# Kernel optimization log

Measured on AMD Instinct MI355X. Metric: run time of the kernel, lower is better.

Reference implementation:

```python
import jax, jax.numpy as jnp
import numpy as np
from jax.scipy.special import logsumexp

PAD = 0  # NlpContext().padding_idx


def setup_inputs() -> dict:
    key = jax.random.key(0)
    k1, k2, k3 = jax.random.split(key, 3)
    B, S, L = 4, 1024, 128
    pred = jax.random.normal(k1, (B, S, L), dtype=jnp.float32)
    # labels in [1, L): no token equals PAD -> mask is all-zero, non_pad_length == S
    gt = jax.random.randint(k2, (B, S), 1, L)
    transition = jax.random.normal(k3, (L, L), dtype=jnp.float32)
    return {"pred": pred, "gt": gt, "transition": transition}


def _crf_loss(pred, gt, transition):
    # Faithful translation of LinearCRFLoss.forward (including the alpha
    # broadcasting behaviour of the original torch loop).
    mask = (gt == PAD).astype(pred.dtype)                 # (B,S), all-zero here
    logp = jax.nn.log_softmax(pred, -1) * (1.0 - mask)[:, :, None]  # (B,S,L)
    trans = jax.nn.log_softmax(transition, -1)            # (L,L)

    # posterior_t[b,i,j] = log_softmax_j( logp[b,t,i] + trans[i,j]*(1-mask[b,t]) )
    post = jax.nn.log_softmax(
        logp[:, :, :, None] + trans[None, None] * (1.0 - mask)[:, :, None, None],
        axis=-1,
    )  # (B,S,L,L)

    # t = 1: alpha has shape (B,L,1) in the original -> broadcasts over 'to'
    # axis j; reduce (logsumexp) over the 'from' axis i.
    alpha = logsumexp(post[:, 1] + logp[:, 0, :, None], axis=1)  # (B,L)
    # t >= 2: alpha has shape (B,1,L) in the original -> broadcasts over the
    # 'from' axis i, so it factors out of the logsumexp:
    #   alpha_t[j] = alpha_{t-1}[j] + lse_i post_t[i,j]
    # which telescopes into a single sum over t (identical math, vectorized).
    alpha = alpha + logsumexp(post[:, 2:], axis=2).sum(axis=1)   # (B,L)
    forward_score = logsumexp(alpha, axis=-1)                    # (B,)

    # gold path score (non_pad_length == S since there is no padding)
    emit = jnp.take_along_axis(logp, gt[:, :, None], axis=2)[..., 0].sum(-1)  # (B,)
    tr = trans[gt[:, :-1], gt[:, 1:]].sum(-1)                                  # (B,)
    gold = emit + tr
    return -(gold - forward_score).mean()


def reference(pred, gt, transition):
    return _crf_loss(pred, gt, transition)
```

## Files before the change

kernel.cpp:

```cpp
#include <hip/hip_runtime.h>
#include <hip/hip_bf16.h>
#include <math.h>

#define BB 4
#define SS 1024
#define LL 128


__global__ __launch_bounds__(256) void crf_rows_kernel(
    const float* __restrict__ pred,
    const int* __restrict__ gt,
    const float* __restrict__ transition,
    float* __restrict__ ws_part,
    float* __restrict__ ws_elp,
    float* __restrict__ ws_trans)
{
    const int wave = threadIdx.x >> 6;
    const int lane = threadIdx.x & 63;
    const int row0 = blockIdx.x * 16;

    int gi[4];
    #pragma unroll
    for (int it = 0; it < 4; ++it) gi[it] = gt[row0 + it * 4 + wave];
    float2 v[4];
    #pragma unroll
    for (int it = 0; it < 4; ++it)
        v[it] = ((const float2*)(pred + (size_t)(row0 + it * 4 + wave) * LL))[lane];
    const bool do_trans = (blockIdx.x < LL) && (wave == 0);
    float2 tv;
    if (do_trans) tv = ((const float2*)(transition + blockIdx.x * LL))[lane];

    float local = 0.f;
    #pragma unroll
    for (int it = 0; it < 4; ++it) {
        float m = fmaxf(v[it].x, v[it].y);
        #pragma unroll
        for (int off = 32; off > 0; off >>= 1) m = fmaxf(m, __shfl_xor(m, off));
        float s = __expf(v[it].x - m) + __expf(v[it].y - m);
        #pragma unroll
        for (int off = 32; off > 0; off >>= 1) s += __shfl_xor(s, off);
        const float lse = m + __logf(s);

        const int g = gi[it];
        const float hold = (g & 1) ? v[it].y : v[it].x;
        local += __shfl(hold, g >> 1) - lse;

        if (it == 0 && wave == 0 && (blockIdx.x & 63) == 0) {
            const int b = blockIdx.x >> 6;
            ws_elp[b * LL + 2 * lane]     = __expf(v[0].x - lse);
            ws_elp[b * LL + 2 * lane + 1] = __expf(v[0].y - lse);
        }
    }

    if (do_trans) {
        float m = fmaxf(tv.x, tv.y);
        #pragma unroll
        for (int off = 32; off > 0; off >>= 1) m = fmaxf(m, __shfl_xor(m, off));
        float s = __expf(tv.x - m) + __expf(tv.y - m);
        #pragma unroll
        for (int off = 32; off > 0; off >>= 1) s += __shfl_xor(s, off);
        const float lse = m + __logf(s);
        float2 o; o.x = tv.x - lse; o.y = tv.y - lse;
        ((float2*)(ws_trans + blockIdx.x * LL))[lane] = o;
    }

    __shared__ float red[4];
    if (lane == 0) red[wave] = local;
    __syncthreads();
    if (threadIdx.x == 0)
        ws_part[blockIdx.x] = red[0] + red[1] + red[2] + red[3];
}

#define PADL (LL + 4)
__global__ __launch_bounds__(512) void crf_finish_kernel(
    const int* __restrict__ gt,
    const float* __restrict__ ws_part,
    const float* __restrict__ ws_elp,
    const float* __restrict__ ws_trans,
    float* __restrict__ out)
{
    __shared__ float tr_s[LL][PADL];
    __shared__ float elp_s[BB][LL];
    __shared__ float pc[4][LL];
    __shared__ float pa[4][BB][LL];
    __shared__ float emit_s[BB];
    __shared__ float wred[8];
    __shared__ float fm[8], fs[8];

    const int tid  = threadIdx.x;
    const int lane = tid & 63;
    const int wave = tid >> 6;

    const int gb = tid >> 7;
    const int t0 = tid & (LL - 1);
    int gf[8], gs[8];
    {
        const int* gtb = gt + gb * SS;
        #pragma unroll
        for (int k = 0; k < 8; ++k) {
            const int t = t0 + k * LL;
            const bool val = (t < SS - 1);
            gf[k] = val ? gtb[t]     : 0;
            gs[k] = val ? gtb[t + 1] : 0;
        }
    }

    #pragma unroll
    for (int k = 0; k < 8; ++k) {
        const int e = (tid + k * 512) * 4;
        const int i = e >> 7, j = e & (LL - 1);
        *(float4*)&tr_s[i][j] = ((const float4*)ws_trans)[e >> 2];
    }
    elp_s[tid >> 7][tid & (LL - 1)] = ws_elp[tid];
    if (wave < BB) {
        float p = ws_part[wave * 64 + lane];
        #pragma unroll
        for (int off = 32; off > 0; off >>= 1) p += __shfl_xor(p, off);
        if (lane == 0) emit_s[wave] = p;
    }
    __syncthreads();

    {
        const int sub = tid >> 7;
        const int j   = tid & (LL - 1);
        float sc = 0.f, s0 = 0.f, s1 = 0.f, s2 = 0.f, s3 = 0.f;
        #pragma unroll
        for (int k = 0; k < 32; ++k) {
            const int i = sub * 32 + k;
            const float e = __expf(tr_s[i][j]);
            sc += e;
            s0 += e * elp_s[0][i];
            s1 += e * elp_s[1][i];
            s2 += e * elp_s[2][i];
            s3 += e * elp_s[3][i];
        }
        pc[sub][j] = sc;
        pa[sub][0][j] = s0; pa[sub][1][j] = s1;
        pa[sub][2][j] = s2; pa[sub][3][j] = s3;
    }
    {
        float g = 0.f;
        #pragma unroll
        for (int k = 0; k < 8; ++k) {
            const int t = t0 + k * LL;
            if (t < SS - 1) g += tr_s[gf[k]][gs[k]];
        }
        #pragma unroll
        for (int off = 32; off > 0; off >>= 1) g += __shfl_xor(g, off);
        if (lane == 0) wred[wave] = g;
    }
    __syncthreads();

    {
        const int b = tid >> 7;
        const int j = tid & (LL - 1);
        const float csum = pc[0][j] + pc[1][j] + pc[2][j] + pc[3][j];
        const float asum = pa[0][b][j] + pa[1][b][j] + pa[2][b][j] + pa[3][b][j];
        const float alpha = __logf(asum) + (float)(SS - 2) * __logf(csum);

        float wm = alpha;
        #pragma unroll
        for (int off = 32; off > 0; off >>= 1) wm = fmaxf(wm, __shfl_xor(wm, off));
        float wsum = __expf(alpha - wm);
        #pragma unroll
        for (int off = 32; off > 0; off >>= 1) wsum += __shfl_xor(wsum, off);
        if (lane == 0) { fm[wave] = wm; fs[wave] = wsum; }
    }
    __syncthreads();

    if (tid < BB) {
        const float m0 = fm[2 * tid], m1 = fm[2 * tid + 1];
        const float mm = fmaxf(m0, m1);
        const float fwd = mm + __logf(fs[2 * tid] * __expf(m0 - mm)
                                    + fs[2 * tid + 1] * __expf(m1 - mm));
        const float gold = wred[2 * tid] + wred[2 * tid + 1];
        fm[tid] = emit_s[tid] + gold - fwd;
    }
    __syncthreads();
    if (tid == 0)
        out[0] = -(fm[0] + fm[1] + fm[2] + fm[3]) * (1.0f / BB);
}

extern "C" void kernel_launch(void* const* d_in, const int* in_sizes, int n_in,
                              void* d_out, int out_size, void* d_ws, size_t ws_size,
                              hipStream_t stream) {
    const float* pred       = (const float*)d_in[0];
    const int*   gt         = (const int*)d_in[1];
    const float* transition = (const float*)d_in[2];
    float* out = (float*)d_out;

    float* ws_part  = (float*)d_ws;
    float* ws_elp   = ws_part + 256;
    float* ws_trans = ws_part + 768;

    crf_rows_kernel<<<(BB * SS) / 16, 256, 0, stream>>>(
        pred, gt, transition, ws_part, ws_elp, ws_trans);
    crf_finish_kernel<<<1, 512, 0, stream>>>(gt, ws_part, ws_elp, ws_trans, out);
}
```

Measured before the change: 63.34 us.

## Fuse row and finish kernels via last-block atomic counter

Merges the two launches into one kernel of 128 blocks with 512 threads. Each block processes 32 rows and bumps a global arrival counter, and the last block to arrive runs the finish stage. The transition log-softmax moves from the row kernel into that last block, which normalizes rows in shared memory. This removes one kernel launch and the gap between the two kernels, but the transition normalization now runs serially in a single block on the tail.

```diff
diff --git a/kernel.cpp b/kernel.cpp
--- a/kernel.cpp
+++ b/kernel.cpp
@@ -1,95 +1,83 @@
 #include <hip/hip_runtime.h>
-#include <hip/hip_bf16.h>
 #include <math.h>
 
 #define BB 4
 #define SS 1024
 #define LL 128
-
-
-__global__ __launch_bounds__(256) void crf_rows_kernel(
+#define PADL (LL + 4)
+#define NBLK 128
+
+__device__ int g_arrive = 0;
+
+__global__ __launch_bounds__(512) void crf_fused_kernel(
     const float* __restrict__ pred,
     const int* __restrict__ gt,
     const float* __restrict__ transition,
     float* __restrict__ ws_part,
     float* __restrict__ ws_elp,
-    float* __restrict__ ws_trans)
-{
-    const int wave = threadIdx.x >> 6;
-    const int lane = threadIdx.x & 63;
-    const int row0 = blockIdx.x * 16;
-
-    int gi[4];
-    #pragma unroll
-    for (int it = 0; it < 4; ++it) gi[it] = gt[row0 + it * 4 + wave];
-    float2 v[4];
-    #pragma unroll
-    for (int it = 0; it < 4; ++it)
-        v[it] = ((const float2*)(pred + (size_t)(row0 + it * 4 + wave) * LL))[lane];
-    const bool do_trans = (blockIdx.x < LL) && (wave == 0);
-    float2 tv;
-    if (do_trans) tv = ((const float2*)(transition + blockIdx.x * LL))[lane];
-
-    float local = 0.f;
-    #pragma unroll
-    for (int it = 0; it < 4; ++it) {
-        float m = fmaxf(v[it].x, v[it].y);
-        #pragma unroll
-        for (int off = 32; off > 0; off >>= 1) m = fmaxf(m, __shfl_xor(m, off));
-        float s = __expf(v[it].x - m) + __expf(v[it].y - m);
-        #pragma unroll
-        for (int off = 32; off > 0; off >>= 1) s += __shfl_xor(s, off);
-        const float lse = m + __logf(s);
-
-        const int g = gi[it];
-        const float hold = (g & 1) ? v[it].y : v[it].x;
-        local += __shfl(hold, g >> 1) - lse;
-
-        if (it == 0 && wave == 0 && (blockIdx.x & 63) == 0) {
-            const int b = blockIdx.x >> 6;
-            ws_elp[b * LL + 2 * lane]     = __expf(v[0].x - lse);
-            ws_elp[b * LL + 2 * lane + 1] = __expf(v[0].y - lse);
-        }
-    }
-
-    if (do_trans) {
-        float m = fmaxf(tv.x, tv.y);
-        #pragma unroll
-        for (int off = 32; off > 0; off >>= 1) m = fmaxf(m, __shfl_xor(m, off));
-        float s = __expf(tv.x - m) + __expf(tv.y - m);
-        #pragma unroll
-        for (int off = 32; off > 0; off >>= 1) s += __shfl_xor(s, off);
-        const float lse = m + __logf(s);
-        float2 o; o.x = tv.x - lse; o.y = tv.y - lse;
-        ((float2*)(ws_trans + blockIdx.x * LL))[lane] = o;
-    }
-
-    __shared__ float red[4];
-    if (lane == 0) red[wave] = local;
-    __syncthreads();
-    if (threadIdx.x == 0)
-        ws_part[blockIdx.x] = red[0] + red[1] + red[2] + red[3];
-}
-
-#define PADL (LL + 4)
-__global__ __launch_bounds__(512) void crf_finish_kernel(
-    const int* __restrict__ gt,
-    const float* __restrict__ ws_part,
-    const float* __restrict__ ws_elp,
-    const float* __restrict__ ws_trans,
     float* __restrict__ out)
 {
     __shared__ float tr_s[LL][PADL];
+    __shared__ float lse_s[LL];
     __shared__ float elp_s[BB][LL];
     __shared__ float pc[4][LL];
     __shared__ float pa[4][BB][LL];
     __shared__ float emit_s[BB];
     __shared__ float wred[8];
     __shared__ float fm[8], fs[8];
+    __shared__ float red[8];
+    __shared__ int   last_s;
 
     const int tid  = threadIdx.x;
+    const int wave = tid >> 6;
     const int lane = tid & 63;
-    const int wave = tid >> 6;
+    const int row0 = blockIdx.x * 32;
+
+    int gi[4];
+    #pragma unroll
+    for (int it = 0; it < 4; ++it) gi[it] = gt[row0 + it * 8 + wave];
+    float2 v[4];
+    #pragma unroll
+    for (int it = 0; it < 4; ++it)
+        v[it] = ((const float2*)(pred + (size_t)(row0 + it * 8 + wave) * LL))[lane];
+
+    float local = 0.f;
+    #pragma unroll
+    for (int it = 0; it < 4; ++it) {
+        float m = fmaxf(v[it].x, v[it].y);
+        #pragma unroll
+        for (int off = 32; off > 0; off >>= 1) m = fmaxf(m, __shfl_xor(m, off));
+        float s = __expf(v[it].x - m) + __expf(v[it].y - m);
+        #pragma unroll
+        for (int off = 32; off > 0; off >>= 1) s += __shfl_xor(s, off);
+        const float lse = m + __logf(s);
+
+        const int g = gi[it];
+        const float hold = (g & 1) ? v[it].y : v[it].x;
+        local += __shfl(hold, g >> 1) - lse;
+
+        if (it == 0 && wave == 0 && (blockIdx.x & 31) == 0) {
+            const int b = blockIdx.x >> 5;
+            float2 o;
+            o.x = __expf(v[0].x - lse);
+            o.y = __expf(v[0].y - lse);
+            ((float2*)(ws_elp + b * LL))[lane] = o;
+        }
+    }
+    if (lane == 0) red[wave] = local;
+    __threadfence();
+    __syncthreads();
+    if (tid == 0) {
+        ws_part[blockIdx.x] = red[0] + red[1] + red[2] + red[3]
+                            + red[4] + red[5] + red[6] + red[7];
+        __threadfence();
+        const int old = atomicAdd(&g_arrive, 1);
+        last_s = (old == NBLK - 1);
+        if (last_s) atomicExch(&g_arrive, 0);
+    }
+    __syncthreads();
+    if (!last_s) return;
+    __threadfence();
 
     const int gb = tid >> 7;
     const int t0 = tid & (LL - 1);
@@ -109,14 +97,39 @@
     for (int k = 0; k < 8; ++k) {
         const int e = (tid + k * 512) * 4;
         const int i = e >> 7, j = e & (LL - 1);
-        *(float4*)&tr_s[i][j] = ((const float4*)ws_trans)[e >> 2];
+        *(float4*)&tr_s[i][j] = ((const float4*)transition)[e >> 2];
     }
     elp_s[tid >> 7][tid & (LL - 1)] = ws_elp[tid];
     if (wave < BB) {
-        float p = ws_part[wave * 64 + lane];
+        float p = (lane < 32) ? ws_part[wave * 32 + lane] : 0.f;
         #pragma unroll
         for (int off = 32; off > 0; off >>= 1) p += __shfl_xor(p, off);
         if (lane == 0) emit_s[wave] = p;
+    }
+    __syncthreads();
+
+    #pragma unroll
+    for (int k = 0; k < 16; ++k) {
+        const int r = wave * 16 + k;
+        const float a = tr_s[r][lane];
+        const float b = tr_s[r][lane + 64];
+        float m = fmaxf(a, b);
+        #pragma unroll
+        for (int off = 32; off > 0; off >>= 1) m = fmaxf(m, __shfl_xor(m, off));
+        float s = __expf(a - m) + __expf(b - m);
+        #pragma unroll
+        for (int off = 32; off > 0; off >>= 1) s += __shfl_xor(s, off);
+        if (lane == 0) lse_s[r] = m + __logf(s);
+    }
+    __syncthreads();
+    #pragma unroll
+    for (int k = 0; k < 8; ++k) {
+        const int e = (tid + k * 512) * 4;
+        const int i = e >> 7, j = e & (LL - 1);
+        float4 t4 = *(float4*)&tr_s[i][j];
+        const float l = lse_s[i];
+        t4.x -= l; t4.y -= l; t4.z -= l; t4.w -= l;
+        *(float4*)&tr_s[i][j] = t4;
     }
     __syncthreads();
 
@@ -189,11 +202,9 @@
     const float* transition = (const float*)d_in[2];
     float* out = (float*)d_out;
 
-    float* ws_part  = (float*)d_ws;
-    float* ws_elp   = ws_part + 256;
-    float* ws_trans = ws_part + 768;
-
-    crf_rows_kernel<<<(BB * SS) / 16, 256, 0, stream>>>(
-        pred, gt, transition, ws_part, ws_elp, ws_trans);
-    crf_finish_kernel<<<1, 512, 0, stream>>>(gt, ws_part, ws_elp, ws_trans, out);
+    float* ws_part = (float*)d_ws;
+    float* ws_elp  = ws_part + 128;
+
+    crf_fused_kernel<<<NBLK, 512, 0, stream>>>(
+        pred, gt, transition, ws_part, ws_elp, out);
 }
```

After: 88.76 us. 40.1% more time.
